# Optimization experiments

Hardware: AMD Instinct MI355X
Metric: run time of the kernel (lower is better)

The kernel has to match this reference:

```python
import jax, jax.numpy as jnp
import numpy as np

B, L, D = 2, 4096, 1024
H = 8
DK = D // H          # 128 head qk dim (expand_k=1)
DV = 2 * D // H      # 256 head v dim (expand_v=2)
FFN = 4 * D          # 4096
CHUNK = 64
EPS = 1e-6


def _ln(x, w, b):
    mu = x.mean(-1, keepdims=True)
    var = ((x - mu) ** 2).mean(-1, keepdims=True)
    return (x - mu) / jnp.sqrt(var + EPS) * w + b


def _retention(q, k, v):
    # q,k: [B,H,L,DK], v: [B,H,L,DV]; RetNet decayed causal linear attention,
    # computed chunkwise (intra-chunk parallel + inter-chunk recurrent state).
    Bq, Hq, Lq, Dk = q.shape
    Dv = v.shape[-1]
    N = Lq // CHUNK
    b = 1.0 - jnp.exp2(-5.0 - jnp.arange(Hq, dtype=q.dtype))   # [H] per-head decay
    logb = jnp.log(b)
    q = q * (Dk ** -0.5)
    t = jnp.arange(CHUNK, dtype=q.dtype)
    diff = t[:, None] - t[None, :]                              # [C,C]
    mask = jnp.where(diff >= 0, jnp.exp(logb[:, None, None] * diff), 0.0)  # [H,C,C]
    d_q = jnp.exp(logb[:, None] * (t[None, :] + 1.0))           # b^(t+1), [H,C]
    d_k = jnp.exp(logb[:, None] * (CHUNK - 1.0 - t[None, :]))   # b^(C-1-s), [H,C]
    d_c = jnp.exp(logb * CHUNK)                                 # b^C, [H]

    def to_chunks(x):
        return x.reshape(Bq, Hq, N, CHUNK, -1).transpose(2, 0, 1, 3, 4)  # [N,B,H,C,d]

    qc, kc, vc = to_chunks(q), to_chunks(k), to_chunks(v)
    S0 = jnp.zeros((Bq, Hq, Dk, Dv), q.dtype)

    def step(S, inp):
        qi, ki, vi = inp                                        # [B,H,C,*]
        A = jnp.einsum('bhtd,bhsd->bhts', qi, ki) * mask        # intra-chunk scores
        o = jnp.einsum('bhts,bhsv->bhtv', A, vi)
        o = o + jnp.einsum('bhtd,bhdv->bhtv', qi * d_q[None, :, :, None], S)
        S = S * d_c[None, :, None, None] + jnp.einsum('bhsd,bhsv->bhdv', ki * d_k[None, :, :, None], vi)
        return S, o

    _, os = jax.lax.scan(step, S0, (qc, kc, vc))                # os: [N,B,H,C,DV]
    return os.transpose(1, 2, 0, 3, 4).reshape(Bq, Hq, Lq, Dv)


def setup_inputs() -> dict:
    key = jax.random.key(0)
    ks = jax.random.split(key, 8)
    s = 0.02
    return {
        'x': jax.random.normal(ks[0], (B, L, D), jnp.float32),
        'ln1_w': jnp.ones((D,), jnp.float32),
        'ln1_b': jnp.zeros((D,), jnp.float32),
        'Wq': jax.random.normal(ks[1], (D, D), jnp.float32) * s,
        'Wk': jax.random.normal(ks[2], (D, D), jnp.float32) * s,
        'Wv': jax.random.normal(ks[3], (D, 2 * D), jnp.float32) * s,
        'Wo': jax.random.normal(ks[4], (2 * D, D), jnp.float32) * s,
        'ln2_w': jnp.ones((D,), jnp.float32),
        'ln2_b': jnp.zeros((D,), jnp.float32),
        'W1': jax.random.normal(ks[5], (D, FFN), jnp.float32) * s,
        'b1': jnp.zeros((FFN,), jnp.float32),
        'W2': jax.random.normal(ks[6], (FFN, D), jnp.float32) * s,
        'b2': jnp.zeros((D,), jnp.float32),
    }


def reference(x, ln1_w, ln1_b, Wq, Wk, Wv, Wo, ln2_w, ln2_b, W1, b1, W2, b2):
    # retention branch
    h = _ln(x, ln1_w, ln1_b)
    q = (h @ Wq).reshape(B, L, H, DK).transpose(0, 2, 1, 3)
    k = (h @ Wk).reshape(B, L, H, DK).transpose(0, 2, 1, 3)
    v = (h @ Wv).reshape(B, L, H, DV).transpose(0, 2, 1, 3)
    o = _retention(q, k, v)                                      # [B,H,L,DV]
    o = o.transpose(0, 2, 1, 3).reshape(B, L, H * DV)
    x = x + o @ Wo
    # FFN branch (exact gelu, no subln, eval-mode dropout)
    f = _ln(x, ln2_w, ln2_b)
    f = jax.nn.gelu(f @ W1 + b1, approximate=False)
    x = x + (f @ W2 + b2)
    return x
```

## Files before the change

### kernel.cpp

```cpp
#include <hip/hip_runtime.h>
#include <math.h>

typedef short s16;
typedef __attribute__((ext_vector_type(8))) short short8;
typedef __attribute__((ext_vector_type(4))) float f32x4;

__device__ __forceinline__ float bf2f_lo(unsigned u){ return __builtin_bit_cast(float, u << 16); }
__device__ __forceinline__ float bf2f_hi(unsigned u){ return __builtin_bit_cast(float, u & 0xffff0000u); }
__device__ __forceinline__ float bf2f(unsigned short h){ return __builtin_bit_cast(float, (unsigned)h << 16); }
__device__ __forceinline__ s16 f2bf(float f){
  unsigned u = __builtin_bit_cast(unsigned, f);
  u += 0x7fffu + ((u >> 16) & 1u);
  return (s16)(u >> 16);
}
__device__ __forceinline__ void unpack8(int4 v, float* f){
  unsigned a=(unsigned)v.x, b=(unsigned)v.y, c=(unsigned)v.z, d=(unsigned)v.w;
  f[0]=bf2f_lo(a); f[1]=bf2f_hi(a); f[2]=bf2f_lo(b); f[3]=bf2f_hi(b);
  f[4]=bf2f_lo(c); f[5]=bf2f_hi(c); f[6]=bf2f_lo(d); f[7]=bf2f_hi(d);
}
__device__ __forceinline__ void gl2lds16(const s16* g, s16* l){
  __builtin_amdgcn_global_load_lds((const __attribute__((address_space(1))) void*)g,
                                   (__attribute__((address_space(3))) void*)l, 16, 0, 0);
}

__global__ __launch_bounds__(256) void ln_bf16(const float* __restrict__ x,
                                               const float* __restrict__ w,
                                               const float* __restrict__ b,
                                               s16* __restrict__ out){
  int row = blockIdx.x; int t = threadIdx.x;
  const float* xr = x + (size_t)row * 1024;
  float4 v = *(const float4*)(xr + t*4);
  float s = v.x + v.y + v.z + v.w;
  float ss = v.x*v.x + v.y*v.y + v.z*v.z + v.w*v.w;
  for (int o = 32; o > 0; o >>= 1){ s += __shfl_down(s, o, 64); ss += __shfl_down(ss, o, 64); }
  __shared__ float red[8];
  int wid = t >> 6, lane = t & 63;
  if (lane == 0){ red[wid] = s; red[4+wid] = ss; }
  __syncthreads();
  if (t == 0){
    float S = red[0]+red[1]+red[2]+red[3];
    float SS = red[4]+red[5]+red[6]+red[7];
    red[0] = S * (1.f/1024.f);
    red[1] = SS * (1.f/1024.f);
  }
  __syncthreads();
  float mu = red[0];
  float var = red[1] - mu*mu;
  float rstd = rsqrtf(var + 1e-6f);
  float vv[4] = {v.x, v.y, v.z, v.w};
  short4 o4;
  s16 tmp[4];
  #pragma unroll
  for (int i = 0; i < 4; ++i){
    int c = t*4 + i;
    float val = (vv[i] - mu) * rstd * w[c] + b[c];
    tmp[i] = f2bf(val);
  }
  o4.x = tmp[0]; o4.y = tmp[1]; o4.z = tmp[2]; o4.w = tmp[3];
  *(short4*)(out + (size_t)row*1024 + t*4) = o4;
}

__global__ __launch_bounds__(256) void conv_t(const float* __restrict__ W,
                                              s16* __restrict__ Wt,
                                              int K, int N, float scale){
  __shared__ float tile[32][33];
  int n0 = blockIdx.x * 32, k0 = blockIdx.y * 32;
  int tx = threadIdx.x & 31, ty = threadIdx.x >> 5;
  #pragma unroll
  for (int i = 0; i < 4; ++i){
    int r = ty + i*8;
    tile[r][tx] = W[(size_t)(k0 + r)*N + n0 + tx];
  }
  __syncthreads();
  #pragma unroll
  for (int i = 0; i < 4; ++i){
    int r = ty + i*8;
    Wt[(size_t)(n0 + r)*K + k0 + tx] = f2bf(tile[tx][r] * scale);
  }
}

__device__ __forceinline__ void xcd_tile(int tiles_y, int& tx, int& ty){
  int id = blockIdx.x;
  int sy = tiles_y >> 3;
  int xcd = id & 7, p = id >> 3;
  ty = xcd * sy + (p % sy);
  tx = p / sy;
}

#define VMW(n) asm volatile("s_waitcnt vmcnt(" #n ")" ::: "memory")
#define BARR() asm volatile("s_barrier" ::: "memory")

__global__ __launch_bounds__(512,2) void gemm256(const s16* __restrict__ A,
                                                 const s16* __restrict__ Bt,
                                                 int N, int K,
                                                 s16* __restrict__ Cb,
                                                 const float* __restrict__ bias,
                                                 int flags, int tiles_y){
  __shared__ s16 lds[2*4*8192];
  int t = threadIdx.x;
  int tx, ty; xcd_tile(tiles_y, tx, ty);
  int m0 = ty * 256, n0 = tx * 256;
  int w = t >> 6, lane = t & 63;
  int wm = w >> 2, wn = w & 3;
  int lrow = lane & 15, lq = lane >> 4;
  int s = lrow & 7;

  int grow = t >> 3;
  int g = (t & 7) ^ (grow & 7);
  int wo = w * 512;

  const s16* pA0 = A  + (size_t)(m0 + grow) * K + g*8;
  const s16* pA1 = pA0 + (size_t)64*K;
  const s16* pA2 = pA0 + (size_t)128*K;
  const s16* pA3 = pA0 + (size_t)192*K;
  const s16* pB0 = Bt + (size_t)(n0 + grow) * K + g*8;
  const s16* pB1 = pB0 + (size_t)64*K;
  const s16* pB2 = pB0 + (size_t)128*K;
  const s16* pB3 = pB0 + (size_t)192*K;

  int abase = (wm*64 + lrow) * 64;
  int bbase = (wn*32 + lrow) * 64;
  int sw0 = ((lq ^ s) << 3);
  int sw1 = (((4 + lq) ^ s) << 3);

  const s16* rA0s0 = lds + abase + sw0;
  const s16* rA0s1 = lds + abase + sw1;
  const s16* rA1s0 = lds + 4*8192 + abase + sw0;
  const s16* rA1s1 = lds + 4*8192 + abase + sw1;
  const s16* rB0s0 = lds + 2*8192 + bbase + sw0;
  const s16* rB0s1 = lds + 2*8192 + bbase + sw1;
  const s16* rB1s0 = lds + 6*8192 + bbase + sw0;
  const s16* rB1s1 = lds + 6*8192 + bbase + sw1;

  f32x4 acc[2][4][2][2];
  #pragma unroll
  for (int a = 0; a < 2; ++a)
    #pragma unroll
    for (int b = 0; b < 4; ++b)
      #pragma unroll
      for (int c = 0; c < 2; ++c)
        #pragma unroll
        for (int d = 0; d < 2; ++d) acc[a][b][c][d] = (f32x4){0.f,0.f,0.f,0.f};

  short8 af[2][4];
  short8 bf0[2][2], bf1[2][2];

#define STGA0(buf) do{ gl2lds16(pA0, lds+((buf)*4+0)*8192+wo); gl2lds16(pA1, lds+((buf)*4+0)*8192+4096+wo); pA0+=64; pA1+=64; }while(0)
#define STGA1(buf) do{ gl2lds16(pA2, lds+((buf)*4+1)*8192+wo); gl2lds16(pA3, lds+((buf)*4+1)*8192+4096+wo); pA2+=64; pA3+=64; }while(0)
#define STGB0(buf) do{ gl2lds16(pB0, lds+((buf)*4+2)*8192+wo); gl2lds16(pB1, lds+((buf)*4+2)*8192+4096+wo); pB0+=64; pB1+=64; }while(0)
#define STGB1(buf) do{ gl2lds16(pB2, lds+((buf)*4+3)*8192+wo); gl2lds16(pB3, lds+((buf)*4+3)*8192+4096+wo); pB2+=64; pB3+=64; }while(0)
#define RDAF(buf,mh) do{ _Pragma("unroll") for (int m_ = 0; m_ < 4; ++m_){ \
    af[0][m_] = *(const short8*)(rA##buf##s0 + (mh)*8192 + m_*1024); \
    af[1][m_] = *(const short8*)(rA##buf##s1 + (mh)*8192 + m_*1024); } }while(0)
#define RDBF(buf,nh,dst) do{ _Pragma("unroll") for (int n_ = 0; n_ < 2; ++n_){ \
    dst[0][n_] = *(const short8*)(rB##buf##s0 + (nh)*8192 + n_*1024); \
    dst[1][n_] = *(const short8*)(rB##buf##s1 + (nh)*8192 + n_*1024); } }while(0)
#define MFMA_Q(mh,nh,B_) do{ __builtin_amdgcn_s_setprio(1); \
    _Pragma("unroll") for (int kk_ = 0; kk_ < 2; ++kk_) \
      _Pragma("unroll") for (int m_ = 0; m_ < 4; ++m_) \
        _Pragma("unroll") for (int n_ = 0; n_ < 2; ++n_) \
          acc[mh][m_][nh][n_] = __builtin_amdgcn_mfma_f32_16x16x32_bf16( \
              af[kk_][m_], B_[kk_][n_], acc[mh][m_][nh][n_], 0, 0, 0); \
    __builtin_amdgcn_s_setprio(0); }while(0)

  int NT = K >> 6;
  STGA0(0); STGB0(0); STGB1(0); STGA1(0);
  STGA0(1); STGB0(1); STGB1(1);
  VMW(6); BARR();
  RDAF(0,0); RDBF(0,0,bf0);

  for (int it = 0; it < (NT-2)/2; ++it){
    STGA1(1); BARR(); MFMA_Q(0,0,bf0); RDBF(0,1,bf1);
    STGA0(0); BARR(); MFMA_Q(0,1,bf1); RDAF(0,1);
    STGB0(0); BARR(); MFMA_Q(1,0,bf0);
    STGB1(0); VMW(6); BARR(); MFMA_Q(1,1,bf1); RDAF(1,0); RDBF(1,0,bf0);
    STGA1(0); BARR(); MFMA_Q(0,0,bf0); RDBF(1,1,bf1);
    STGA0(1); BARR(); MFMA_Q(0,1,bf1); RDAF(1,1);
    STGB0(1); BARR(); MFMA_Q(1,0,bf0);
    STGB1(1); VMW(6); BARR(); MFMA_Q(1,1,bf1); RDAF(0,0); RDBF(0,0,bf0);
  }
  {
    STGA1(1);
    BARR(); MFMA_Q(0,0,bf0); RDBF(0,1,bf1);
    BARR(); MFMA_Q(0,1,bf1); RDAF(0,1);
    BARR(); MFMA_Q(1,0,bf0);
    VMW(0); BARR(); MFMA_Q(1,1,bf1); RDAF(1,0); RDBF(1,0,bf0);
    BARR(); MFMA_Q(0,0,bf0); RDBF(1,1,bf1);
    BARR(); MFMA_Q(0,1,bf1); RDAF(1,1);
    BARR(); MFMA_Q(1,0,bf0);
    MFMA_Q(1,1,bf1);
  }
#undef STGA0
#undef STGA1
#undef STGB0
#undef STGB1
#undef RDAF
#undef RDBF
#undef MFMA_Q

  bool do_gelu = flags & 1;
  #pragma unroll
  for (int nh = 0; nh < 2; ++nh){
    #pragma unroll
    for (int nj = 0; nj < 2; ++nj){
      int col = n0 + wn*32 + nh*128 + nj*16 + lrow;
      float bcol = bias ? bias[col] : 0.f;
      #pragma unroll
      for (int mh = 0; mh < 2; ++mh){
        #pragma unroll
        for (int m = 0; m < 4; ++m){
          int row_base = m0 + wm*64 + mh*128 + m*16 + lq*4;
          #pragma unroll
          for (int r = 0; r < 4; ++r){
            float val = acc[mh][m][nh][nj][r] + bcol;
            if (do_gelu) val = 0.5f * val * (1.f + erff(val * 0.70710678118654752f));
            Cb[(size_t)(row_base + r) * N + col] = f2bf(val);
          }
        }
      }
    }
  }
}

__global__ __launch_bounds__(512,2) void gemm256h(const s16* __restrict__ A,
                                                  const s16* __restrict__ Bt,
                                                  int N, int K,
                                                  float* __restrict__ Cf,
                                                  s16* __restrict__ Cb,
                                                  const float* __restrict__ bias,
                                                  const float* __restrict__ resid,
                                                  int flags, int tiles_y){
  __shared__ s16 lds[2*3*8192];
  int t = threadIdx.x;
  int tx, ty; xcd_tile(tiles_y, tx, ty);
  int m0 = ty * 256, n0 = tx * 128;
  int w = t >> 6, lane = t & 63;
  int wm = w >> 2, wn = w & 3;
  int lrow = lane & 15, lq = lane >> 4;
  int s = lrow & 7;

  int grow = t >> 3;
  int g = (t & 7) ^ (grow & 7);
  int wo = w * 512;

  const s16* pA0 = A  + (size_t)(m0 + grow) * K + g*8;
  const s16* pA1 = pA0 + (size_t)64*K;
  const s16* pA2 = pA0 + (size_t)128*K;
  const s16* pA3 = pA0 + (size_t)192*K;
  const s16* pB0 = Bt + (size_t)(n0 + grow) * K + g*8;
  const s16* pB1 = pB0 + (size_t)64*K;

  int abase = (wm*64 + lrow) * 64;
  int bbase = (wn*32 + lrow) * 64;
  int sw0 = ((lq ^ s) << 3);
  int sw1 = (((4 + lq) ^ s) << 3);

  const s16* rA0s0 = lds + abase + sw0;
  const s16* rA0s1 = lds + abase + sw1;
  const s16* rA1s0 = lds + 3*8192 + abase + sw0;
  const s16* rA1s1 = lds + 3*8192 + abase + sw1;
  const s16* rB0s0 = lds + 2*8192 + bbase + sw0;
  const s16* rB0s1 = lds + 2*8192 + bbase + sw1;
  const s16* rB1s0 = lds + 5*8192 + bbase + sw0;
  const s16* rB1s1 = lds + 5*8192 + bbase + sw1;

  f32x4 acc[2][4][2];
  #pragma unroll
  for (int a = 0; a < 2; ++a)
    #pragma unroll
    for (int b = 0; b < 4; ++b)
      #pragma unroll
      for (int c = 0; c < 2; ++c) acc[a][b][c] = (f32x4){0.f,0.f,0.f,0.f};

  short8 af[2][4];
  short8 bfE[2][2], bfO[2][2];

#define STGHA0(buf) do{ gl2lds16(pA0, lds+((buf)*3+0)*8192+wo); gl2lds16(pA1, lds+((buf)*3+0)*8192+4096+wo); pA0+=64; pA1+=64; }while(0)
#define STGHA1(buf) do{ gl2lds16(pA2, lds+((buf)*3+1)*8192+wo); gl2lds16(pA3, lds+((buf)*3+1)*8192+4096+wo); pA2+=64; pA3+=64; }while(0)
#define STGHB(buf)  do{ gl2lds16(pB0, lds+((buf)*3+2)*8192+wo); gl2lds16(pB1, lds+((buf)*3+2)*8192+4096+wo); pB0+=64; pB1+=64; }while(0)
#define RDAH(buf,mh) do{ _Pragma("unroll") for (int m_ = 0; m_ < 4; ++m_){ \
    af[0][m_] = *(const short8*)(rA##buf##s0 + (mh)*8192 + m_*1024); \
    af[1][m_] = *(const short8*)(rA##buf##s1 + (mh)*8192 + m_*1024); } }while(0)
#define RDBH(buf,dst) do{ _Pragma("unroll") for (int n_ = 0; n_ < 2; ++n_){ \
    dst[0][n_] = *(const short8*)(rB##buf##s0 + n_*1024); \
    dst[1][n_] = *(const short8*)(rB##buf##s1 + n_*1024); } }while(0)
#define MFMA_H(mh,B_) do{ __builtin_amdgcn_s_setprio(1); \
    _Pragma("unroll") for (int kk_ = 0; kk_ < 2; ++kk_) \
      _Pragma("unroll") for (int m_ = 0; m_ < 4; ++m_) \
        _Pragma("unroll") for (int n_ = 0; n_ < 2; ++n_) \
          acc[mh][m_][n_] = __builtin_amdgcn_mfma_f32_16x16x32_bf16( \
              af[kk_][m_], B_[kk_][n_], acc[mh][m_][n_], 0, 0, 0); \
    __builtin_amdgcn_s_setprio(0); }while(0)

  int NT = K >> 6;
  STGHA0(0); STGHB(0); STGHA1(0);
  STGHA0(1); STGHB(1);
  VMW(4); BARR();
  RDAH(0,0); RDBH(0,bfE);

  for (int it = 0; it < (NT-2)/2; ++it){
    STGHA1(1);
    BARR(); MFMA_H(0,bfE); RDAH(0,1);
    STGHA0(0); STGHB(0);
    VMW(4);
    BARR(); MFMA_H(1,bfE); RDAH(1,0); RDBH(1,bfO);
    STGHA1(0);
    BARR(); MFMA_H(0,bfO); RDAH(1,1);
    STGHA0(1); STGHB(1);
    VMW(4);
    BARR(); MFMA_H(1,bfO); RDAH(0,0); RDBH(0,bfE);
  }
  {
    STGHA1(1);
    BARR(); MFMA_H(0,bfE); RDAH(0,1);
    VMW(0);
    BARR(); MFMA_H(1,bfE); RDAH(1,0); RDBH(1,bfO);
    BARR(); MFMA_H(0,bfO); RDAH(1,1);
    MFMA_H(1,bfO);
  }
#undef STGHA0
#undef STGHA1
#undef STGHB
#undef RDAH
#undef RDBH
#undef MFMA_H

  bool do_gelu = flags & 1;
  bool out_bf = flags & 2;
  #pragma unroll
  for (int nj = 0; nj < 2; ++nj){
    int col = n0 + wn*32 + nj*16 + lrow;
    float bcol = bias ? bias[col] : 0.f;
    #pragma unroll
    for (int mh = 0; mh < 2; ++mh){
      #pragma unroll
      for (int m = 0; m < 4; ++m){
        int row_base = m0 + wm*64 + mh*128 + m*16 + lq*4;
        #pragma unroll
        for (int r = 0; r < 4; ++r){
          int grow_ = row_base + r;
          float val = acc[mh][m][nj][r] + bcol;
          if (do_gelu) val = 0.5f * val * (1.f + erff(val * 0.70710678118654752f));
          if (resid) val += resid[(size_t)grow_ * N + col];
          if (out_bf) Cb[(size_t)grow_ * N + col] = f2bf(val);
          else        Cf[(size_t)grow_ * N + col] = val;
        }
      }
    }
  }
}

__global__ __launch_bounds__(256,2) void ret_chunksum(const s16* __restrict__ k,
                                                      const s16* __restrict__ v,
                                                      s16* __restrict__ U){
  int bi = blockIdx.x;
  int h = bi & 7, n = bi >> 3;
  int t = threadIdx.x;
  __shared__ s16 ks[128*72];
  __shared__ s16 vs[256*72];
  float log2b = log2f(1.f - exp2f(-5.f - (float)h));
  const s16* kbase = k + (size_t)(n*64)*4096 + h*128;
  const s16* vbase = v + (size_t)(n*64)*4096 + h*256;
  #pragma unroll
  for (int i = 0; i < 4; ++i){
    int e = i*2048 + t*8;
    int s = e >> 7, dk = e & 127;
    int4 kv = *(const int4*)(kbase + (size_t)s*4096 + dk);
    float f[8]; unpack8(kv, f);
    float dec = exp2f(log2b * (float)(63 - s));
    #pragma unroll
    for (int j = 0; j < 8; ++j) ks[(dk+j)*72 + s] = f2bf(f[j]*dec);
  }
  #pragma unroll
  for (int i = 0; i < 8; ++i){
    int e = i*2048 + t*8;
    int s = e >> 8, dv = e & 255;
    int4 vv = *(const int4*)(vbase + (size_t)s*4096 + dv);
    s16 tmp[8]; *(int4*)tmp = vv;
    #pragma unroll
    for (int j = 0; j < 8; ++j) vs[(dv+j)*72 + s] = tmp[j];
  }
  __syncthreads();
  int w = t >> 6, lane = t & 63;
  int m0w = w*64;
  int lrow = lane & 15, lq = lane >> 4;
  f32x4 acc[4][8];
  #pragma unroll
  for (int mi = 0; mi < 4; ++mi)
    #pragma unroll
    for (int ni = 0; ni < 8; ++ni) acc[mi][ni] = (f32x4){0.f,0.f,0.f,0.f};
  #pragma unroll
  for (int kk = 0; kk < 64; kk += 32){
    short8 af[4], bfr[8];
    #pragma unroll
    for (int mi = 0; mi < 4; ++mi)
      af[mi] = *(short8*)&vs[(m0w + mi*16 + lrow)*72 + kk + lq*8];
    #pragma unroll
    for (int ni = 0; ni < 8; ++ni)
      bfr[ni] = *(short8*)&ks[(ni*16 + lrow)*72 + kk + lq*8];
    #pragma unroll
    for (int mi = 0; mi < 4; ++mi)
      #pragma unroll
      for (int ni = 0; ni < 8; ++ni)
        acc[mi][ni] = __builtin_amdgcn_mfma_f32_16x16x32_bf16(af[mi], bfr[ni], acc[mi][ni], 0, 0, 0);
  }
  s16* Ub = U + ((size_t)(h*64 + n))*32768;
  #pragma unroll
  for (int mi = 0; mi < 4; ++mi)
    #pragma unroll
    for (int ni = 0; ni < 8; ++ni)
      #pragma unroll
      for (int r = 0; r < 4; ++r){
        int row = m0w + mi*16 + lq*4 + r;
        int col = ni*16 + lrow;
        Ub[(size_t)row*128 + col] = f2bf(acc[mi][ni][r]);
      }
}

__global__ __launch_bounds__(256) void ret_scan(s16* __restrict__ US){
  int tid = blockIdx.x*256 + threadIdx.x;
  int h = tid >> 12;
  int rem = tid & 4095;
  int dv = rem >> 4, dk0 = (rem & 15)*8;
  float log2b = log2f(1.f - exp2f(-5.f - (float)h));
  float dc = exp2f(log2b * 64.f);
  s16* base = US + (size_t)h*64*32768 + (size_t)dv*128 + dk0;
  float acc[8] = {0.f,0.f,0.f,0.f,0.f,0.f,0.f,0.f};
  #pragma unroll 4
  for (int n = 0; n < 64; ++n){
    s16* p = base + (size_t)n*32768;
    int4 u4 = *(const int4*)p;
    float uf[8]; unpack8(u4, uf);
    s16 sb[8];
    #pragma unroll
    for (int j = 0; j < 8; ++j) sb[j] = f2bf(acc[j]);
    *(int4*)p = *(int4*)sb;
    #pragma unroll
    for (int j = 0; j < 8; ++j) acc[j] = acc[j]*dc + uf[j];
  }
}

__global__ __launch_bounds__(256,2) void ret_attn(const s16* __restrict__ q,
                                                  const s16* __restrict__ k,
                                                  const s16* __restrict__ v,
                                                  const s16* __restrict__ S,
                                                  s16* __restrict__ o){
  int bi = blockIdx.x;
  int h = bi & 7, n = bi >> 3;
  int t = threadIdx.x;
  int w = t >> 6, lane = t & 63;
  int lrow = lane & 15, lq = lane >> 4;
  float log2b = log2f(1.f - exp2f(-5.f - (float)h));
  __shared__ s16 As[64*72];
  __shared__ s16 vs[256*72];

  const s16* vbase = v + (size_t)(n*64)*4096 + h*256;
  #pragma unroll
  for (int i = 0; i < 8; ++i){
    int e = i*2048 + t*8;
    int s = e >> 8, dv = e & 255;
    int4 vv = *(const int4*)(vbase + (size_t)s*4096 + dv);
    s16 tmp[8]; *(int4*)tmp = vv;
    #pragma unroll
    for (int j = 0; j < 8; ++j) vs[(dv+j)*72 + s] = tmp[j];
  }

  const s16* qbase = q + (size_t)(n*64)*4096 + h*128;
  const s16* kbase = k + (size_t)(n*64)*4096 + h*128;
  short8 qf[4][4];
  #pragma unroll
  for (int ti = 0; ti < 4; ++ti)
    #pragma unroll
    for (int c = 0; c < 4; ++c)
      qf[ti][c] = *(const short8*)(qbase + (size_t)(ti*16 + lrow)*4096 + c*32 + lq*8);
  short8 kf[4];
  #pragma unroll
  for (int c = 0; c < 4; ++c)
    kf[c] = *(const short8*)(kbase + (size_t)(16*w + lrow)*4096 + c*32 + lq*8);
  #pragma unroll
  for (int ti = 0; ti < 4; ++ti){
    f32x4 acc_a = (f32x4){0.f,0.f,0.f,0.f};
    #pragma unroll
    for (int c = 0; c < 4; ++c)
      acc_a = __builtin_amdgcn_mfma_f32_16x16x32_bf16(qf[ti][c], kf[c], acc_a, 0, 0, 0);
    #pragma unroll
    for (int r = 0; r < 4; ++r){
      int ti_idx = ti*16 + lq*4 + r;
      int s_idx = 16*w + lrow;
      int d = ti_idx - s_idx;
      float val = (d >= 0) ? acc_a[r] * exp2f(log2b * (float)d) : 0.f;
      As[ti_idx*72 + s_idx] = f2bf(val);
    }
  }
  __syncthreads();

  f32x4 acc[4][4];
  #pragma unroll
  for (int mi = 0; mi < 4; ++mi)
    #pragma unroll
    for (int nj = 0; nj < 4; ++nj) acc[mi][nj] = (f32x4){0.f,0.f,0.f,0.f};

  const s16* Sbase = S + ((size_t)(h*64 + n)*256 + w*64)*128;
  #pragma unroll
  for (int c = 0; c < 4; ++c){
    short8 bf[4];
    #pragma unroll
    for (int nj = 0; nj < 4; ++nj)
      bf[nj] = *(const short8*)(Sbase + (size_t)(nj*16 + lrow)*128 + c*32 + lq*8);
    #pragma unroll
    for (int mi = 0; mi < 4; ++mi)
      #pragma unroll
      for (int nj = 0; nj < 4; ++nj)
        acc[mi][nj] = __builtin_amdgcn_mfma_f32_16x16x32_bf16(qf[mi][c], bf[nj], acc[mi][nj], 0, 0, 0);
  }
  #pragma unroll
  for (int mi = 0; mi < 4; ++mi){
    #pragma unroll
    for (int r = 0; r < 4; ++r){
      float dq = exp2f(log2b * (float)(mi*16 + lq*4 + r + 1));
      #pragma unroll
      for (int nj = 0; nj < 4; ++nj) acc[mi][nj][r] *= dq;
    }
  }
  #pragma unroll
  for (int c = 0; c < 2; ++c){
    short8 af[4], bf[4];
    #pragma unroll
    for (int mi = 0; mi < 4; ++mi)
      af[mi] = *(short8*)&As[(mi*16 + lrow)*72 + c*32 + lq*8];
    #pragma unroll
    for (int nj = 0; nj < 4; ++nj)
      bf[nj] = *(short8*)&vs[(w*64 + nj*16 + lrow)*72 + c*32 + lq*8];
    #pragma unroll
    for (int mi = 0; mi < 4; ++mi)
      #pragma unroll
      for (int nj = 0; nj < 4; ++nj)
        acc[mi][nj] = __builtin_amdgcn_mfma_f32_16x16x32_bf16(af[mi], bf[nj], acc[mi][nj], 0, 0, 0);
  }
  s16* obase = o + (size_t)(n*64)*2048 + h*256;
  #pragma unroll
  for (int mi = 0; mi < 4; ++mi)
    #pragma unroll
    for (int nj = 0; nj < 4; ++nj)
      #pragma unroll
      for (int r = 0; r < 4; ++r){
        int row = mi*16 + lq*4 + r;
        int col = w*64 + nj*16 + lrow;
        obase[(size_t)row*2048 + col] = f2bf(acc[mi][nj][r]);
      }
}

extern "C" void kernel_launch(void* const* d_in, const int* in_sizes, int n_in,
                              void* d_out, int out_size, void* d_ws, size_t ws_size,
                              hipStream_t stream) {
  (void)in_sizes; (void)n_in; (void)out_size; (void)ws_size;
  const float* x     = (const float*)d_in[0];
  const float* ln1_w = (const float*)d_in[1];
  const float* ln1_b = (const float*)d_in[2];
  const float* Wq    = (const float*)d_in[3];
  const float* Wk    = (const float*)d_in[4];
  const float* Wv    = (const float*)d_in[5];
  const float* Wo    = (const float*)d_in[6];
  const float* ln2_w = (const float*)d_in[7];
  const float* ln2_b = (const float*)d_in[8];
  const float* W1    = (const float*)d_in[9];
  const float* b1    = (const float*)d_in[10];
  const float* W2    = (const float*)d_in[11];
  const float* b2    = (const float*)d_in[12];
  float* out = (float*)d_out;
  char* ws = (char*)d_ws;

  const size_t MB = 1ull << 20;
  s16* Wqkv_t = (s16*)(ws + 0*MB);
  s16* Wo_t = (s16*)(ws + 8*MB);
  s16* W1_t = (s16*)(ws + 12*MB);
  s16* W2_t = (s16*)(ws + 20*MB);
  s16* hbuf = (s16*)(ws + 28*MB);
  s16* h2   = (s16*)(ws + 28*MB);
  s16* qkv  = (s16*)(ws + 44*MB);
  float* x1 = (float*)(ws + 44*MB);
  s16* fb   = (s16*)(ws + 76*MB);
  s16* US   = (s16*)(ws + 108*MB);
  s16* ob   = (s16*)(ws + 140*MB);

  conv_t<<<dim3(32,32),  256, 0, stream>>>(Wq, Wqkv_t, 1024, 1024, 0.08838834764831845f);
  conv_t<<<dim3(32,32),  256, 0, stream>>>(Wk, Wqkv_t + (size_t)1024*1024, 1024, 1024, 1.f);
  conv_t<<<dim3(64,32),  256, 0, stream>>>(Wv, Wqkv_t + (size_t)2048*1024, 1024, 2048, 1.f);
  conv_t<<<dim3(32,64),  256, 0, stream>>>(Wo, Wo_t, 2048, 1024, 1.f);
  conv_t<<<dim3(128,32), 256, 0, stream>>>(W1, W1_t, 1024, 4096, 1.f);
  conv_t<<<dim3(32,128), 256, 0, stream>>>(W2, W2_t, 4096, 1024, 1.f);

  ln_bf16<<<8192, 256, 0, stream>>>(x, ln1_w, ln1_b, hbuf);

  gemm256<<<512, 512, 0, stream>>>(hbuf, Wqkv_t, 4096, 1024, qkv, nullptr, 0, 32);

  for (int b = 0; b < 2; ++b){
    const s16* q_b = qkv + (size_t)b*4096*4096;
    const s16* k_b = q_b + 1024;
    const s16* v_b = q_b + 2048;
    s16* ob_b = ob + (size_t)b*4096*2048;
    ret_chunksum<<<512, 256, 0, stream>>>(k_b, v_b, US);
    ret_scan<<<128, 256, 0, stream>>>(US);
    ret_attn<<<512, 256, 0, stream>>>(q_b, k_b, v_b, US, ob_b);
  }

  gemm256h<<<256, 512, 0, stream>>>(ob, Wo_t, 1024, 2048, x1, nullptr, nullptr, x, 0, 32);
  ln_bf16<<<8192, 256, 0, stream>>>(x1, ln2_w, ln2_b, h2);

  gemm256<<<512, 512, 0, stream>>>(h2, W1_t, 4096, 1024, fb, b1, 1, 32);
  gemm256h<<<256, 512, 0, stream>>>(fb, W2_t, 1024, 4096, out, nullptr, b2, x1, 0, 32);
}
```

Measured before the change: 615.9 us.

## Restructure GEMM main loops into ping-pong phases with explicit LDS waits and barriers

Both GEMM kernels (256x256 and the half-tile variant) are rewritten around TILE macros. Each phase now issues its LDS fragment reads and global-to-LDS stages, then barriers and waits on lgkmcnt(0) before the MFMA cluster, with a second barrier after it. This replaces the earlier scheme where reads for the next quarter were issued after each MFMA block. The intent is a ping-pong style schedule that separates memory phases from MFMA phases across the two waves per SIMD. It also frees registers, since one B fragment buffer replaces two in the half kernel. The cost is twice as many barriers and a full LDS wait before each MFMA block.

```diff
diff --git a/kernel.cpp b/kernel.cpp
--- a/kernel.cpp
+++ b/kernel.cpp
@@ -89,6 +89,7 @@
 
 #define VMW(n) asm volatile("s_waitcnt vmcnt(" #n ")" ::: "memory")
 #define BARR() asm volatile("s_barrier" ::: "memory")
+#define LGKM0() asm volatile("s_waitcnt lgkmcnt(0)" ::: "memory")
 
 __global__ __launch_bounds__(512,2) void gemm256(const s16* __restrict__ A,
                                                  const s16* __restrict__ Bt,
@@ -163,33 +164,43 @@
               af[kk_][m_], B_[kk_][n_], acc[mh][m_][nh][n_], 0, 0, 0); \
     __builtin_amdgcn_s_setprio(0); }while(0)
 
+#define TILE(c,n) do{ \
+     RDAF(c,0); RDBF(c,0,bf0); STGA1(n); \
+    BARR(); LGKM0(); MFMA_Q(0,0,bf0); BARR(); \
+     RDBF(c,1,bf1); STGA0(c); \
+    BARR(); LGKM0(); MFMA_Q(0,1,bf1); BARR(); \
+     RDAF(c,1); STGB0(c); \
+    BARR(); LGKM0(); MFMA_Q(1,0,bf0); BARR(); \
+     STGB1(c); VMW(6); \
+    BARR(); MFMA_Q(1,1,bf1); BARR(); }while(0)
+
   int NT = K >> 6;
   STGA0(0); STGB0(0); STGB1(0); STGA1(0);
   STGA0(1); STGB0(1); STGB1(1);
   VMW(6); BARR();
-  RDAF(0,0); RDBF(0,0,bf0);
 
   for (int it = 0; it < (NT-2)/2; ++it){
-    STGA1(1); BARR(); MFMA_Q(0,0,bf0); RDBF(0,1,bf1);
-    STGA0(0); BARR(); MFMA_Q(0,1,bf1); RDAF(0,1);
-    STGB0(0); BARR(); MFMA_Q(1,0,bf0);
-    STGB1(0); VMW(6); BARR(); MFMA_Q(1,1,bf1); RDAF(1,0); RDBF(1,0,bf0);
-    STGA1(0); BARR(); MFMA_Q(0,0,bf0); RDBF(1,1,bf1);
-    STGA0(1); BARR(); MFMA_Q(0,1,bf1); RDAF(1,1);
-    STGB0(1); BARR(); MFMA_Q(1,0,bf0);
-    STGB1(1); VMW(6); BARR(); MFMA_Q(1,1,bf1); RDAF(0,0); RDBF(0,0,bf0);
+    TILE(0,1);
+    TILE(1,0);
   }
   {
-    STGA1(1);
-    BARR(); MFMA_Q(0,0,bf0); RDBF(0,1,bf1);
-    BARR(); MFMA_Q(0,1,bf1); RDAF(0,1);
-    BARR(); MFMA_Q(1,0,bf0);
-    VMW(0); BARR(); MFMA_Q(1,1,bf1); RDAF(1,0); RDBF(1,0,bf0);
-    BARR(); MFMA_Q(0,0,bf0); RDBF(1,1,bf1);
-    BARR(); MFMA_Q(0,1,bf1); RDAF(1,1);
-    BARR(); MFMA_Q(1,0,bf0);
+    RDAF(0,0); RDBF(0,0,bf0); STGA1(1);
+    BARR(); LGKM0(); MFMA_Q(0,0,bf0); BARR();
+    RDBF(0,1,bf1);
+    BARR(); LGKM0(); MFMA_Q(0,1,bf1); BARR();
+    RDAF(0,1);
+    BARR(); LGKM0(); MFMA_Q(1,0,bf0); BARR();
+    VMW(0);
+    BARR(); MFMA_Q(1,1,bf1); BARR();
+    RDAF(1,0); RDBF(1,0,bf0);
+    BARR(); LGKM0(); MFMA_Q(0,0,bf0); BARR();
+    RDBF(1,1,bf1);
+    BARR(); LGKM0(); MFMA_Q(0,1,bf1); BARR();
+    RDAF(1,1);
+    LGKM0(); MFMA_Q(1,0,bf0);
     MFMA_Q(1,1,bf1);
   }
+#undef TILE
 #undef STGA0
 #undef STGA1
 #undef STGB0
@@ -273,7 +284,7 @@
       for (int c = 0; c < 2; ++c) acc[a][b][c] = (f32x4){0.f,0.f,0.f,0.f};
 
   short8 af[2][4];
-  short8 bfE[2][2], bfO[2][2];
+  short8 bf[2][2];
 
 #define STGHA0(buf) do{ gl2lds16(pA0, lds+((buf)*3+0)*8192+wo); gl2lds16(pA1, lds+((buf)*3+0)*8192+4096+wo); pA0+=64; pA1+=64; }while(0)
 #define STGHA1(buf) do{ gl2lds16(pA2, lds+((buf)*3+1)*8192+wo); gl2lds16(pA3, lds+((buf)*3+1)*8192+4096+wo); pA2+=64; pA3+=64; }while(0)
@@ -281,43 +292,44 @@
 #define RDAH(buf,mh) do{ _Pragma("unroll") for (int m_ = 0; m_ < 4; ++m_){ \
     af[0][m_] = *(const short8*)(rA##buf##s0 + (mh)*8192 + m_*1024); \
     af[1][m_] = *(const short8*)(rA##buf##s1 + (mh)*8192 + m_*1024); } }while(0)
-#define RDBH(buf,dst) do{ _Pragma("unroll") for (int n_ = 0; n_ < 2; ++n_){ \
-    dst[0][n_] = *(const short8*)(rB##buf##s0 + n_*1024); \
-    dst[1][n_] = *(const short8*)(rB##buf##s1 + n_*1024); } }while(0)
-#define MFMA_H(mh,B_) do{ __builtin_amdgcn_s_setprio(1); \
+#define RDBH(buf) do{ _Pragma("unroll") for (int n_ = 0; n_ < 2; ++n_){ \
+    bf[0][n_] = *(const short8*)(rB##buf##s0 + n_*1024); \
+    bf[1][n_] = *(const short8*)(rB##buf##s1 + n_*1024); } }while(0)
+#define MFMA_H(mh) do{ __builtin_amdgcn_s_setprio(1); \
     _Pragma("unroll") for (int kk_ = 0; kk_ < 2; ++kk_) \
       _Pragma("unroll") for (int m_ = 0; m_ < 4; ++m_) \
         _Pragma("unroll") for (int n_ = 0; n_ < 2; ++n_) \
           acc[mh][m_][n_] = __builtin_amdgcn_mfma_f32_16x16x32_bf16( \
-              af[kk_][m_], B_[kk_][n_], acc[mh][m_][n_], 0, 0, 0); \
+              af[kk_][m_], bf[kk_][n_], acc[mh][m_][n_], 0, 0, 0); \
     __builtin_amdgcn_s_setprio(0); }while(0)
+
+#define TILEH(c,n) do{ \
+     RDAH(c,0); RDBH(c); STGHA1(n); \
+    BARR(); LGKM0(); MFMA_H(0); BARR(); \
+     RDAH(c,1); STGHA0(c); STGHB(c); VMW(4); \
+    BARR(); LGKM0(); MFMA_H(1); BARR(); }while(0)
 
   int NT = K >> 6;
   STGHA0(0); STGHB(0); STGHA1(0);
   STGHA0(1); STGHB(1);
   VMW(4); BARR();
-  RDAH(0,0); RDBH(0,bfE);
 
   for (int it = 0; it < (NT-2)/2; ++it){
-    STGHA1(1);
-    BARR(); MFMA_H(0,bfE); RDAH(0,1);
-    STGHA0(0); STGHB(0);
-    VMW(4);
-    BARR(); MFMA_H(1,bfE); RDAH(1,0); RDBH(1,bfO);
-    STGHA1(0);
-    BARR(); MFMA_H(0,bfO); RDAH(1,1);
-    STGHA0(1); STGHB(1);
-    VMW(4);
-    BARR(); MFMA_H(1,bfO); RDAH(0,0); RDBH(0,bfE);
+    TILEH(0,1);
+    TILEH(1,0);
   }
   {
-    STGHA1(1);
-    BARR(); MFMA_H(0,bfE); RDAH(0,1);
+    RDAH(0,0); RDBH(0); STGHA1(1);
+    BARR(); LGKM0(); MFMA_H(0); BARR();
+    RDAH(0,1);
     VMW(0);
-    BARR(); MFMA_H(1,bfE); RDAH(1,0); RDBH(1,bfO);
-    BARR(); MFMA_H(0,bfO); RDAH(1,1);
-    MFMA_H(1,bfO);
-  }
+    BARR(); LGKM0(); MFMA_H(1); BARR();
+    RDAH(1,0); RDBH(1);
+    BARR(); LGKM0(); MFMA_H(0); BARR();
+    RDAH(1,1);
+    LGKM0(); MFMA_H(1);
+  }
+#undef TILEH
 #undef STGHA0
 #undef STGHA1
 #undef STGHB
```

Measured after the change: 628.3 us. 2.0% more time.
